# Kernel optimization log

Hardware: AMD Instinct MI355X
Metric: run time of the kernel (lower is better)

The kernel has to match this reference:

```python
import jax, jax.numpy as jnp
import numpy as np

B, T, C, H = 8, 2048, 1024, 128  # batch, seq (== block_size), embed dim, head size


def setup_inputs() -> dict:
    key = jax.random.key(0)
    kx, kq, kk, kv = jax.random.split(key, 4)
    x = jax.random.normal(kx, (B, T, C), dtype=jnp.float32)
    # torch Linear(no bias) weights: [head_size, in_features], applied as x @ W.T
    s = 1.0 / np.sqrt(C)
    Wq = jax.random.normal(kq, (H, C), dtype=jnp.float32) * s
    Wk = jax.random.normal(kk, (H, C), dtype=jnp.float32) * s
    Wv = jax.random.normal(kv, (H, C), dtype=jnp.float32) * s
    return {"x": x, "Wq": Wq, "Wk": Wk, "Wv": Wv}


def reference(x, Wq, Wk, Wv):
    # projections: [B,T,C] @ [C,H] -> [B,T,H]
    q = jnp.einsum('btc,hc->bth', x, Wq)
    k = jnp.einsum('btc,hc->bth', x, Wk)
    v = jnp.einsum('btc,hc->bth', x, Wv)
    scale = k.shape[-1] ** -0.5
    # scores [B,T,T], causal mask, softmax in fp32 (autocast disabled in original)
    scores = jnp.einsum('bqh,bkh->bqk', q, k) * scale
    causal = jnp.tril(jnp.ones((T, T), dtype=bool))
    scores = jnp.where(causal, scores, -jnp.inf)
    attn = jax.nn.softmax(scores.astype(jnp.float32), axis=-1)
    # dropout_rate = 0.0 -> identity
    out = jnp.einsum('bqk,bkh->bqh', attn.astype(v.dtype), v)
    return out
```

## Files before the change

### kernel.cpp

```cpp
#include <hip/hip_runtime.h>
#include <hip/hip_bf16.h>

constexpr int NB = 8;
constexpr int T  = 2048;
constexpr int C  = 1024;
constexpr int Hd = 128;

typedef short bf16x8 __attribute__((ext_vector_type(8)));
typedef float floatx4 __attribute__((ext_vector_type(4)));

__device__ __forceinline__ ushort f2bf(float x) {
    return __builtin_bit_cast(ushort, __float2bfloat16(x));
}
__device__ __forceinline__ float bf2f(ushort u) {
    unsigned int x = ((unsigned int)u) << 16;
    return __builtin_bit_cast(float, x);
}
__device__ __forceinline__ void async16(ushort* lds, const ushort* g) {
    __builtin_amdgcn_global_load_lds(
        (const __attribute__((address_space(1))) unsigned int*)g,
        (__attribute__((address_space(3))) unsigned int*)lds, 16, 0, 0);
}

__global__ __launch_bounds__(256) void convert_xw(
    const float* __restrict__ X, const float* __restrict__ Wq,
    const float* __restrict__ Wk, const float* __restrict__ Wv,
    ushort* __restrict__ Xb, ushort* __restrict__ Wb)
{
    int bid = blockIdx.x;
    if (bid < 8192) {
        size_t i = ((size_t)bid * 256 + threadIdx.x) * 8;
        float4 a = *(const float4*)&X[i];
        float4 b = *(const float4*)&X[i + 4];
        bf16x8 o;
        o[0] = (short)f2bf(a.x); o[1] = (short)f2bf(a.y);
        o[2] = (short)f2bf(a.z); o[3] = (short)f2bf(a.w);
        o[4] = (short)f2bf(b.x); o[5] = (short)f2bf(b.y);
        o[6] = (short)f2bf(b.z); o[7] = (short)f2bf(b.w);
        *(bf16x8*)&Xb[i] = o;
    } else {
        int g = (bid - 8192) * 256 + threadIdx.x;
        size_t base = (size_t)g * 8;
        int sel = (int)(base >> 17);
        const float* W = sel == 0 ? Wq : (sel == 1 ? Wk : Wv);
        float s = (sel == 0) ? 0.12751744f : 1.0f;
        size_t off = base - (size_t)sel * 131072;
        float4 a = *(const float4*)&W[off];
        float4 b = *(const float4*)&W[off + 4];
        bf16x8 o;
        o[0] = (short)f2bf(a.x * s); o[1] = (short)f2bf(a.y * s);
        o[2] = (short)f2bf(a.z * s); o[3] = (short)f2bf(a.w * s);
        o[4] = (short)f2bf(b.x * s); o[5] = (short)f2bf(b.y * s);
        o[6] = (short)f2bf(b.z * s); o[7] = (short)f2bf(b.w * s);
        *(bf16x8*)&Wb[base] = o;
    }
}

__global__ __launch_bounds__(256) void qkv_gemm(
    const ushort* __restrict__ Xb, const ushort* __restrict__ Wb,
    ushort* __restrict__ Qo, ushort* __restrict__ Ko, ushort* __restrict__ Vt)
{
    __shared__ ushort SM[24576];
    ushort* Al = SM;
    ushort* Bl = SM + 16384;
    const int m0 = blockIdx.x * 128;
    const int n0 = blockIdx.y * 64;
    const int tid = threadIdx.x, lane = tid & 63, wave = tid >> 6;
    const int quad = lane >> 4, colL = lane & 15;
    const int wm = (wave & 1) * 64, wn = (wave >> 1) * 32;
    const int lr4 = lane >> 4;
    const int cg  = lane & 15;

    floatx4 acc[4][2] = {};

    for (int k0 = 0; k0 < C; k0 += 128) {
        for (int t = 0; t < 8; ++t) {
            int q = wave * 8 + t;
            int row = q * 4 + lr4;
            async16(&Al[q * 512 + lane * 8],
                    &Xb[(size_t)(m0 + row) * C + k0 + ((cg ^ (row & 7)) * 8)]);
        }
        for (int t = 0; t < 4; ++t) {
            int q = wave * 4 + t;
            int row = q * 4 + lr4;
            async16(&Bl[q * 512 + lane * 8],
                    &Wb[(size_t)(n0 + row) * C + k0 + ((cg ^ (row & 7)) * 8)]);
        }
        __syncthreads();

        for (int kk = 0; kk < 4; ++kk) {
            bf16x8 af[4], bfr[2];
            for (int mt = 0; mt < 4; ++mt)
                af[mt] = *(const bf16x8*)
                    &Al[(wm + mt * 16 + colL) * 128 + (((kk * 4 + quad) ^ (colL & 7))) * 8];
            for (int nt = 0; nt < 2; ++nt)
                bfr[nt] = *(const bf16x8*)
                    &Bl[(wn + nt * 16 + colL) * 128 + (((kk * 4 + quad) ^ (colL & 7))) * 8];
            for (int mt = 0; mt < 4; ++mt)
                for (int nt = 0; nt < 2; ++nt)
                    acc[mt][nt] = __builtin_amdgcn_mfma_f32_16x16x32_bf16(
                        af[mt], bfr[nt], acc[mt][nt], 0, 0, 0);
        }
        __syncthreads();
    }

    const int sel = n0 >> 7;
    const int h0 = n0 & 127;
    if (sel < 2) {
        ushort* dst = sel == 0 ? Qo : Ko;
        for (int mt = 0; mt < 4; ++mt)
            for (int nt = 0; nt < 2; ++nt)
                for (int r = 0; r < 4; ++r) {
                    int row = m0 + wm + mt * 16 + quad * 4 + r;
                    int h = h0 + wn + nt * 16 + colL;
                    dst[(size_t)row * Hd + h] = f2bf(acc[mt][nt][r]);
                }
    } else {
        ushort* TL = SM;
        for (int mt = 0; mt < 4; ++mt)
            for (int nt = 0; nt < 2; ++nt)
                for (int r = 0; r < 4; ++r)
                    TL[(wm + mt * 16 + quad * 4 + r) * 66 + wn + nt * 16 + colL] =
                        f2bf(acc[mt][nt][r]);
        __syncthreads();
        const int b = m0 >> 11, tb = m0 & 2047;
        const int h = tid & 63, tq = tid >> 6;
        for (int st = 0; st < 4; ++st) {
            int t0 = tq * 32 + st * 8;
            bf16x8 o;
            for (int jx = 0; jx < 8; ++jx)
                o[jx] = (short)TL[(t0 + jx) * 66 + h];
            *(bf16x8*)&Vt[((size_t)b * Hd + h0 + h) * T + tb + t0] = o;
        }
    }
}

__global__ __launch_bounds__(256, 2) void attn_partial(
    const ushort* __restrict__ Q, const ushort* __restrict__ Kg,
    const ushort* __restrict__ Vt, ushort* __restrict__ Opart,
    float* __restrict__ mpart, float* __restrict__ lpart)
{
    __shared__ ushort Kl[128 * 128];
    __shared__ ushort Vl[128 * 128];

    const int tid = threadIdx.x, lane = tid & 63, wave = tid >> 6;
    const int quad = lane >> 4, colL = lane & 15;

    int id = blockIdx.x;
    int b = id / 136;
    int rem = id - b * 136;
    int j = 15;
    while (rem >= j + 1) { rem -= (j + 1); --j; }
    int c = rem;
    const int q0 = j * 128;
    const int k0 = c * 128;
    const bool diag = (c == j);

    {
        int r = tid >> 4, p = tid & 15;
        for (int t = 0; t < 8; ++t) {
            int row = t * 16 + r;
            async16(&Kl[t * 2048 + tid * 8],
                    &Kg[((size_t)b * T + k0 + row) * Hd + ((p ^ (row & 15)) * 8)]);
        }
        for (int t = 0; t < 8; ++t) {
            int hrow = t * 16 + r;
            async16(&Vl[t * 2048 + tid * 8],
                    &Vt[((size_t)b * Hd + hrow) * T + k0 + ((p ^ (hrow & 15)) * 8)]);
        }
    }

    bf16x8 qa[2][4];
    for (int mi = 0; mi < 2; ++mi) {
        const ushort* qp =
            &Q[((size_t)b * T + q0 + wave * 32 + mi * 16 + colL) * Hd + quad * 8];
        for (int ks = 0; ks < 4; ++ks)
            qa[mi][ks] = *(const bf16x8*)&qp[ks * 32];
    }

    __syncthreads();

    floatx4 accS[2][8] = {};
    for (int ks = 0; ks < 4; ++ks)
        for (int nt = 0; nt < 8; ++nt) {
            int krow = nt * 16 + colL;
            bf16x8 kb = *(const bf16x8*)&Kl[krow * 128 + (((ks * 4 + quad) ^ colL) * 8)];
            accS[0][nt] = __builtin_amdgcn_mfma_f32_16x16x32_bf16(qa[0][ks], kb, accS[0][nt], 0, 0, 0);
            accS[1][nt] = __builtin_amdgcn_mfma_f32_16x16x32_bf16(qa[1][ks], kb, accS[1][nt], 0, 0, 0);
        }

    if (diag) {
        for (int mi = 0; mi < 2; ++mi)
            for (int nt = 0; nt < 8; ++nt)
                for (int rr = 0; rr < 4; ++rr) {
                    int lrow = wave * 32 + mi * 16 + quad * 4 + rr;
                    int lcol = nt * 16 + colL;
                    if (lcol > lrow) accS[mi][nt][rr] = -__builtin_inff();
                }
    }
    __syncthreads();

    ushort* Pw = &Kl[wave * 4096];
    float m_r[2][4], l_r[2][4];
    for (int mi = 0; mi < 2; ++mi)
        for (int rr = 0; rr < 4; ++rr) {
            float mx = accS[mi][0][rr];
            for (int nt = 1; nt < 8; ++nt) mx = fmaxf(mx, accS[mi][nt][rr]);
            for (int off = 1; off < 16; off <<= 1)
                mx = fmaxf(mx, __shfl_xor(mx, off, 64));
            m_r[mi][rr] = mx;
            l_r[mi][rr] = 0.f;
        }
    for (int mi = 0; mi < 2; ++mi) {
        for (int nt = 0; nt < 8; ++nt)
            for (int rr = 0; rr < 4; ++rr) {
                float p = __builtin_amdgcn_exp2f(accS[mi][nt][rr] - m_r[mi][rr]);
                l_r[mi][rr] += p;
                int prow = mi * 16 + quad * 4 + rr;
                Pw[prow * 128 + ((nt * 16 + colL) ^ ((prow & 7) << 4))] = f2bf(p);
            }
        for (int rr = 0; rr < 4; ++rr) {
            float s = l_r[mi][rr];
            for (int off = 1; off < 16; off <<= 1)
                s += __shfl_xor(s, off, 64);
            l_r[mi][rr] = s;
        }
    }

    bf16x8 pa[2][4];
    for (int mi = 0; mi < 2; ++mi) {
        int prow = mi * 16 + colL;
        int sw = (prow & 7) << 4;
        for (int ks = 0; ks < 4; ++ks)
            pa[mi][ks] = *(const bf16x8*)&Pw[prow * 128 + ((ks * 32 + quad * 8) ^ sw)];
    }

    floatx4 Oacc[2][8] = {};
    for (int ks = 0; ks < 4; ++ks)
        for (int th = 0; th < 8; ++th) {
            int hrow = th * 16 + colL;
            bf16x8 vb = *(const bf16x8*)&Vl[hrow * 128 + (((ks * 4 + quad) ^ colL) * 8)];
            Oacc[0][th] = __builtin_amdgcn_mfma_f32_16x16x32_bf16(pa[0][ks], vb, Oacc[0][th], 0, 0, 0);
            Oacc[1][th] = __builtin_amdgcn_mfma_f32_16x16x32_bf16(pa[1][ks], vb, Oacc[1][th], 0, 0, 0);
        }

    const int slot = b * 136 + (j * (j + 1)) / 2 + c;
    ushort* Op = &Opart[(size_t)slot * 16384];
    for (int mi = 0; mi < 2; ++mi)
        for (int th = 0; th < 8; ++th)
            for (int rr = 0; rr < 4; ++rr) {
                int row = wave * 32 + mi * 16 + quad * 4 + rr;
                Op[row * 128 + th * 16 + colL] = f2bf(Oacc[mi][th][rr]);
            }
    if (colL == 0)
        for (int mi = 0; mi < 2; ++mi)
            for (int rr = 0; rr < 4; ++rr) {
                int row = wave * 32 + mi * 16 + quad * 4 + rr;
                mpart[(size_t)slot * 128 + row] = m_r[mi][rr];
                lpart[(size_t)slot * 128 + row] = l_r[mi][rr];
            }
}

__global__ __launch_bounds__(256) void attn_combine(
    const ushort* __restrict__ Opart, const float* __restrict__ mpart,
    const float* __restrict__ lpart, float* __restrict__ out)
{
    const int j = blockIdx.x, b = blockIdx.y;
    const int nch = j + 1;
    const int sbase = b * 136 + (j * (j + 1)) / 2;
    const int t = threadIdx.x;
    const int row = blockIdx.z * 32 + (t >> 3);
    const int h0 = (t & 7) * 16;

    float M = -__builtin_inff();
    for (int c = 0; c < nch; ++c)
        M = fmaxf(M, mpart[(size_t)(sbase + c) * 128 + row]);
    float ltot = 0.f;
    for (int c = 0; c < nch; ++c)
        ltot += lpart[(size_t)(sbase + c) * 128 + row] *
                __builtin_amdgcn_exp2f(mpart[(size_t)(sbase + c) * 128 + row] - M);

    float o[16];
    for (int i = 0; i < 16; ++i) o[i] = 0.f;
    for (int c = 0; c < nch; ++c) {
        float wgt = __builtin_amdgcn_exp2f(mpart[(size_t)(sbase + c) * 128 + row] - M);
        const ushort* Op = &Opart[(size_t)(sbase + c) * 16384 + row * 128 + h0];
        for (int x = 0; x < 2; ++x) {
            bf16x8 v = *(const bf16x8*)&Op[x * 8];
            for (int i2 = 0; i2 < 8; ++i2)
                o[x * 8 + i2] += bf2f((ushort)v[i2]) * wgt;
        }
    }
    float inv = 1.0f / ltot;
    float* dst = &out[((size_t)(b * T) + j * 128 + row) * Hd + h0];
    for (int i = 0; i < 16; ++i) dst[i] = o[i] * inv;
}

extern "C" void kernel_launch(void* const* d_in, const int* in_sizes, int n_in,
                              void* d_out, int out_size, void* d_ws, size_t ws_size,
                              hipStream_t stream) {
    const float* x  = (const float*)d_in[0];
    const float* Wq = (const float*)d_in[1];
    const float* Wk = (const float*)d_in[2];
    const float* Wv = (const float*)d_in[3];
    float* out = (float*)d_out;

    char* w = (char*)d_ws;
    ushort* Xb = (ushort*)w;
    ushort* Wb = (ushort*)(w + (size_t)33554432);
    ushort* Opart = (ushort*)w;
    float* mpart = (float*)(w + (size_t)35651584);
    float* lpart = (float*)(w + (size_t)35651584 + 557056);
    w += (size_t)35651584 + 2 * 557056;
    ushort* Qb  = (ushort*)w;  w += (size_t)NB * T * Hd * 2;
    ushort* Kb  = (ushort*)w;  w += (size_t)NB * T * Hd * 2;
    ushort* Vtb = (ushort*)w;  w += (size_t)NB * T * Hd * 2;

    convert_xw<<<8384, 256, 0, stream>>>(x, Wq, Wk, Wv, Xb, Wb);
    qkv_gemm<<<dim3(128, 6), 256, 0, stream>>>(Xb, Wb, Qb, Kb, Vtb);
    attn_partial<<<1088, 256, 0, stream>>>(Qb, Kb, Vtb, Opart, mpart, lpart);
    attn_combine<<<dim3(16, 8, 4), 256, 0, stream>>>(Opart, mpart, lpart, out);
}
```

Baseline: 163.3 us.

## Replace split-KV partial attention and combine with single-pass flash attention kernel

Replaces the per-(query tile, key tile) partial attention kernel and the separate combine kernel with one flash-attention kernel. Each block handles 64 query rows, loops over key tiles with an online softmax, and writes the normalized fp32 output directly. This removes the bf16 partial-output round trip through global memory and one launch. In exchange the grid shrinks to 256 blocks with serial key-tile loops whose lengths vary, and there is no double buffering, so load latency is exposed each iteration.

New measurement: 166.0 us. Within noise of the previous version (+1.7%).

```diff
diff --git a/kernel.cpp b/kernel.cpp
--- a/kernel.cpp
+++ b/kernel.cpp
@@ -135,10 +135,9 @@
     }
 }
 
-__global__ __launch_bounds__(256, 2) void attn_partial(
+__global__ __launch_bounds__(256, 2) void attn_flash(
     const ushort* __restrict__ Q, const ushort* __restrict__ Kg,
-    const ushort* __restrict__ Vt, ushort* __restrict__ Opart,
-    float* __restrict__ mpart, float* __restrict__ lpart)
+    const ushort* __restrict__ Vt, float* __restrict__ out)
 {
     __shared__ ushort Kl[128 * 128];
     __shared__ ushort Vl[128 * 128];
@@ -146,154 +145,114 @@
     const int tid = threadIdx.x, lane = tid & 63, wave = tid >> 6;
     const int quad = lane >> 4, colL = lane & 15;
 
-    int id = blockIdx.x;
-    int b = id / 136;
-    int rem = id - b * 136;
-    int j = 15;
-    while (rem >= j + 1) { rem -= (j + 1); --j; }
-    int c = rem;
-    const int q0 = j * 128;
-    const int k0 = c * 128;
-    const bool diag = (c == j);
-
+    const int id = blockIdx.x;
+    const int b = id & 7;
+    const int qt = 31 - (id >> 3);
+    const int q0 = qt * 64;
+    const int cmax = (q0 + 63) >> 7;
+
+    bf16x8 qa[4];
     {
-        int r = tid >> 4, p = tid & 15;
+        const ushort* qp =
+            &Q[((size_t)b * T + q0 + wave * 16 + colL) * Hd + quad * 8];
+        for (int ks = 0; ks < 4; ++ks)
+            qa[ks] = *(const bf16x8*)&qp[ks * 32];
+    }
+
+    floatx4 Oacc[8] = {};
+    float m_r[4], l_r[4];
+    for (int rr = 0; rr < 4; ++rr) { m_r[rr] = -__builtin_inff(); l_r[rr] = 0.f; }
+
+    const int r16 = tid >> 4, p16 = tid & 15;
+
+    for (int c = 0; c <= cmax; ++c) {
+        if (c > 0) __syncthreads();
+        const int k0 = c * 128;
         for (int t = 0; t < 8; ++t) {
-            int row = t * 16 + r;
+            int row = t * 16 + r16;
             async16(&Kl[t * 2048 + tid * 8],
-                    &Kg[((size_t)b * T + k0 + row) * Hd + ((p ^ (row & 15)) * 8)]);
+                    &Kg[((size_t)b * T + k0 + row) * Hd + ((p16 ^ (row & 15)) * 8)]);
         }
         for (int t = 0; t < 8; ++t) {
-            int hrow = t * 16 + r;
+            int hrow = t * 16 + r16;
             async16(&Vl[t * 2048 + tid * 8],
-                    &Vt[((size_t)b * Hd + hrow) * T + k0 + ((p ^ (hrow & 15)) * 8)]);
-        }
-    }
-
-    bf16x8 qa[2][4];
-    for (int mi = 0; mi < 2; ++mi) {
-        const ushort* qp =
-            &Q[((size_t)b * T + q0 + wave * 32 + mi * 16 + colL) * Hd + quad * 8];
+                    &Vt[((size_t)b * Hd + hrow) * T + k0 + ((p16 ^ (hrow & 15)) * 8)]);
+        }
+        __syncthreads();
+
+        floatx4 accS[8] = {};
         for (int ks = 0; ks < 4; ++ks)
-            qa[mi][ks] = *(const bf16x8*)&qp[ks * 32];
-    }
-
-    __syncthreads();
-
-    floatx4 accS[2][8] = {};
-    for (int ks = 0; ks < 4; ++ks)
-        for (int nt = 0; nt < 8; ++nt) {
-            int krow = nt * 16 + colL;
-            bf16x8 kb = *(const bf16x8*)&Kl[krow * 128 + (((ks * 4 + quad) ^ colL) * 8)];
-            accS[0][nt] = __builtin_amdgcn_mfma_f32_16x16x32_bf16(qa[0][ks], kb, accS[0][nt], 0, 0, 0);
-            accS[1][nt] = __builtin_amdgcn_mfma_f32_16x16x32_bf16(qa[1][ks], kb, accS[1][nt], 0, 0, 0);
-        }
-
-    if (diag) {
-        for (int mi = 0; mi < 2; ++mi)
+            for (int nt = 0; nt < 8; ++nt) {
+                int krow = nt * 16 + colL;
+                bf16x8 kb = *(const bf16x8*)&Kl[krow * 128 + (((ks * 4 + quad) ^ colL) * 8)];
+                accS[nt] = __builtin_amdgcn_mfma_f32_16x16x32_bf16(qa[ks], kb, accS[nt], 0, 0, 0);
+            }
+
+        if (c == cmax) {
             for (int nt = 0; nt < 8; ++nt)
                 for (int rr = 0; rr < 4; ++rr) {
-                    int lrow = wave * 32 + mi * 16 + quad * 4 + rr;
-                    int lcol = nt * 16 + colL;
-                    if (lcol > lrow) accS[mi][nt][rr] = -__builtin_inff();
+                    int lrow = q0 + wave * 16 + quad * 4 + rr;
+                    int lcol = k0 + nt * 16 + colL;
+                    if (lcol > lrow) accS[nt][rr] = -__builtin_inff();
                 }
-    }
-    __syncthreads();
-
-    ushort* Pw = &Kl[wave * 4096];
-    float m_r[2][4], l_r[2][4];
-    for (int mi = 0; mi < 2; ++mi)
+        }
+        __syncthreads();
+
+        float sc[4];
         for (int rr = 0; rr < 4; ++rr) {
-            float mx = accS[mi][0][rr];
-            for (int nt = 1; nt < 8; ++nt) mx = fmaxf(mx, accS[mi][nt][rr]);
+            float mx = accS[0][rr];
+            for (int nt = 1; nt < 8; ++nt) mx = fmaxf(mx, accS[nt][rr]);
             for (int off = 1; off < 16; off <<= 1)
                 mx = fmaxf(mx, __shfl_xor(mx, off, 64));
-            m_r[mi][rr] = mx;
-            l_r[mi][rr] = 0.f;
-        }
-    for (int mi = 0; mi < 2; ++mi) {
-        for (int nt = 0; nt < 8; ++nt)
+            float nm = fmaxf(m_r[rr], mx);
+            sc[rr] = __builtin_amdgcn_exp2f(m_r[rr] - nm);
+            m_r[rr] = nm;
+        }
+        for (int th = 0; th < 8; ++th)
+            for (int rr = 0; rr < 4; ++rr)
+                Oacc[th][rr] *= sc[rr];
+
+        ushort* Pw = &Kl[wave * 2048];
+        {
+            float ls[4] = {0.f, 0.f, 0.f, 0.f};
+            for (int nt = 0; nt < 8; ++nt)
+                for (int rr = 0; rr < 4; ++rr) {
+                    float p = __builtin_amdgcn_exp2f(accS[nt][rr] - m_r[rr]);
+                    ls[rr] += p;
+                    int prow = quad * 4 + rr;
+                    Pw[prow * 128 + ((nt * 16 + colL) ^ ((prow & 7) << 4))] = f2bf(p);
+                }
             for (int rr = 0; rr < 4; ++rr) {
-                float p = __builtin_amdgcn_exp2f(accS[mi][nt][rr] - m_r[mi][rr]);
-                l_r[mi][rr] += p;
-                int prow = mi * 16 + quad * 4 + rr;
-                Pw[prow * 128 + ((nt * 16 + colL) ^ ((prow & 7) << 4))] = f2bf(p);
+                float s = ls[rr];
+                for (int off = 1; off < 16; off <<= 1)
+                    s += __shfl_xor(s, off, 64);
+                l_r[rr] = l_r[rr] * sc[rr] + s;
             }
+        }
+
+        bf16x8 pa[4];
+        {
+            const int prow = colL;
+            const int sw = (prow & 7) << 4;
+            for (int ks = 0; ks < 4; ++ks)
+                pa[ks] = *(const bf16x8*)&Pw[prow * 128 + ((ks * 32 + quad * 8) ^ sw)];
+        }
+
+        for (int ks = 0; ks < 4; ++ks)
+            for (int th = 0; th < 8; ++th) {
+                int hrow = th * 16 + colL;
+                bf16x8 vb = *(const bf16x8*)&Vl[hrow * 128 + (((ks * 4 + quad) ^ colL) * 8)];
+                Oacc[th] = __builtin_amdgcn_mfma_f32_16x16x32_bf16(pa[ks], vb, Oacc[th], 0, 0, 0);
+            }
+    }
+
+    float inv[4];
+    for (int rr = 0; rr < 4; ++rr) inv[rr] = 1.0f / l_r[rr];
+    for (int th = 0; th < 8; ++th)
         for (int rr = 0; rr < 4; ++rr) {
-            float s = l_r[mi][rr];
-            for (int off = 1; off < 16; off <<= 1)
-                s += __shfl_xor(s, off, 64);
-            l_r[mi][rr] = s;
-        }
-    }
-
-    bf16x8 pa[2][4];
-    for (int mi = 0; mi < 2; ++mi) {
-        int prow = mi * 16 + colL;
-        int sw = (prow & 7) << 4;
-        for (int ks = 0; ks < 4; ++ks)
-            pa[mi][ks] = *(const bf16x8*)&Pw[prow * 128 + ((ks * 32 + quad * 8) ^ sw)];
-    }
-
-    floatx4 Oacc[2][8] = {};
-    for (int ks = 0; ks < 4; ++ks)
-        for (int th = 0; th < 8; ++th) {
-            int hrow = th * 16 + colL;
-            bf16x8 vb = *(const bf16x8*)&Vl[hrow * 128 + (((ks * 4 + quad) ^ colL) * 8)];
-            Oacc[0][th] = __builtin_amdgcn_mfma_f32_16x16x32_bf16(pa[0][ks], vb, Oacc[0][th], 0, 0, 0);
-            Oacc[1][th] = __builtin_amdgcn_mfma_f32_16x16x32_bf16(pa[1][ks], vb, Oacc[1][th], 0, 0, 0);
-        }
-
-    const int slot = b * 136 + (j * (j + 1)) / 2 + c;
-    ushort* Op = &Opart[(size_t)slot * 16384];
-    for (int mi = 0; mi < 2; ++mi)
-        for (int th = 0; th < 8; ++th)
-            for (int rr = 0; rr < 4; ++rr) {
-                int row = wave * 32 + mi * 16 + quad * 4 + rr;
-                Op[row * 128 + th * 16 + colL] = f2bf(Oacc[mi][th][rr]);
-            }
-    if (colL == 0)
-        for (int mi = 0; mi < 2; ++mi)
-            for (int rr = 0; rr < 4; ++rr) {
-                int row = wave * 32 + mi * 16 + quad * 4 + rr;
-                mpart[(size_t)slot * 128 + row] = m_r[mi][rr];
-                lpart[(size_t)slot * 128 + row] = l_r[mi][rr];
-            }
-}
-
-__global__ __launch_bounds__(256) void attn_combine(
-    const ushort* __restrict__ Opart, const float* __restrict__ mpart,
-    const float* __restrict__ lpart, float* __restrict__ out)
-{
-    const int j = blockIdx.x, b = blockIdx.y;
-    const int nch = j + 1;
-    const int sbase = b * 136 + (j * (j + 1)) / 2;
-    const int t = threadIdx.x;
-    const int row = blockIdx.z * 32 + (t >> 3);
-    const int h0 = (t & 7) * 16;
-
-    float M = -__builtin_inff();
-    for (int c = 0; c < nch; ++c)
-        M = fmaxf(M, mpart[(size_t)(sbase + c) * 128 + row]);
-    float ltot = 0.f;
-    for (int c = 0; c < nch; ++c)
-        ltot += lpart[(size_t)(sbase + c) * 128 + row] *
-                __builtin_amdgcn_exp2f(mpart[(size_t)(sbase + c) * 128 + row] - M);
-
-    float o[16];
-    for (int i = 0; i < 16; ++i) o[i] = 0.f;
-    for (int c = 0; c < nch; ++c) {
-        float wgt = __builtin_amdgcn_exp2f(mpart[(size_t)(sbase + c) * 128 + row] - M);
-        const ushort* Op = &Opart[(size_t)(sbase + c) * 16384 + row * 128 + h0];
-        for (int x = 0; x < 2; ++x) {
-            bf16x8 v = *(const bf16x8*)&Op[x * 8];
-            for (int i2 = 0; i2 < 8; ++i2)
-                o[x * 8 + i2] += bf2f((ushort)v[i2]) * wgt;
-        }
-    }
-    float inv = 1.0f / ltot;
-    float* dst = &out[((size_t)(b * T) + j * 128 + row) * Hd + h0];
-    for (int i = 0; i < 16; ++i) dst[i] = o[i] * inv;
+            int row = q0 + wave * 16 + quad * 4 + rr;
+            out[((size_t)b * T + row) * Hd + th * 16 + colL] = Oacc[th][rr] * inv[rr];
+        }
 }
 
 extern "C" void kernel_launch(void* const* d_in, const int* in_sizes, int n_in,
@@ -306,18 +265,13 @@
     float* out = (float*)d_out;
 
     char* w = (char*)d_ws;
-    ushort* Xb = (ushort*)w;
-    ushort* Wb = (ushort*)(w + (size_t)33554432);
-    ushort* Opart = (ushort*)w;
-    float* mpart = (float*)(w + (size_t)35651584);
-    float* lpart = (float*)(w + (size_t)35651584 + 557056);
-    w += (size_t)35651584 + 2 * 557056;
+    ushort* Xb = (ushort*)w;  w += (size_t)33554432;
+    ushort* Wb = (ushort*)w;  w += (size_t)786432;
     ushort* Qb  = (ushort*)w;  w += (size_t)NB * T * Hd * 2;
     ushort* Kb  = (ushort*)w;  w += (size_t)NB * T * Hd * 2;
     ushort* Vtb = (ushort*)w;  w += (size_t)NB * T * Hd * 2;
 
     convert_xw<<<8384, 256, 0, stream>>>(x, Wq, Wk, Wv, Xb, Wb);
     qkv_gemm<<<dim3(128, 6), 256, 0, stream>>>(Xb, Wb, Qb, Kb, Vtb);
-    attn_partial<<<1088, 256, 0, stream>>>(Qb, Kb, Vtb, Opart, mpart, lpart);
-    attn_combine<<<dim3(16, 8, 4), 256, 0, stream>>>(Opart, mpart, lpart, out);
-}
+    attn_flash<<<256, 256, 0, stream>>>(Qb, Kb, Vtb, out);
+}
```
